# Performance work log

Hardware: AMD Instinct MI355X
Metric: run time of the kernel (lower is better)

## Reference

```python
import jax, jax.numpy as jnp
import numpy as np

N_NODES = 50000
N_EDGES = 800000
HIDDEN = 128
HEADS = 4
LAYERS = 2
NEG_SLOPE = 0.2


def setup_inputs() -> dict:
    key = jax.random.key(0)
    ks = jax.random.split(key, 12)
    s_in = 1.0 / np.sqrt(HIDDEN)
    x = jax.random.normal(ks[0], (N_NODES, HIDDEN), dtype=jnp.float32)
    edge_index = jax.random.randint(ks[1], (2, N_EDGES), 0, N_NODES, dtype=jnp.int64)
    conv_w = jax.random.normal(ks[2], (LAYERS, HIDDEN, HEADS * HIDDEN), dtype=jnp.float32) * s_in
    att_src = jax.random.normal(ks[3], (LAYERS, HEADS, HIDDEN), dtype=jnp.float32) * s_in
    att_dst = jax.random.normal(ks[4], (LAYERS, HEADS, HIDDEN), dtype=jnp.float32) * s_in
    conv_b = jax.random.normal(ks[5], (LAYERS, HIDDEN), dtype=jnp.float32) * 0.01
    proj_w = jax.random.normal(ks[6], (LAYERS, HIDDEN, HIDDEN), dtype=jnp.float32) * s_in
    proj_b = jax.random.normal(ks[7], (LAYERS, HIDDEN), dtype=jnp.float32) * 0.01
    skip_w = jax.random.normal(ks[8], (LAYERS, HIDDEN, HIDDEN), dtype=jnp.float32) * s_in
    skip_b = jax.random.normal(ks[9], (LAYERS, HIDDEN), dtype=jnp.float32) * 0.01
    return {"x": x, "edge_index": edge_index, "conv_w": conv_w, "att_src": att_src,
            "att_dst": att_dst, "conv_b": conv_b, "proj_w": proj_w, "proj_b": proj_b,
            "skip_w": skip_w, "skip_b": skip_b}


def _gat_layer(x, src, dst, W, a_s, a_d, b):
    # x: [N, D]; W: [D, H*C]; a_s, a_d: [H, C]; b: [C]
    N = x.shape[0]
    h = (x @ W).reshape(N, HEADS, HIDDEN)          # [N, H, C]
    alpha_src = jnp.einsum('nhc,hc->nh', h, a_s)   # [N, H]
    alpha_dst = jnp.einsum('nhc,hc->nh', h, a_d)   # [N, H]
    alpha = alpha_src[src] + alpha_dst[dst]        # [E, H]
    alpha = jnp.where(alpha >= 0, alpha, NEG_SLOPE * alpha)  # leaky_relu(0.2)
    amax = jax.ops.segment_max(alpha, dst, num_segments=N)   # [N, H]
    ex = jnp.exp(alpha - amax[dst])                # [E, H]
    denom = jax.ops.segment_sum(ex, dst, num_segments=N)     # [N, H]
    w = ex / (denom[dst] + 1e-16)                  # PyG softmax eps
    msg = h[src] * w[:, :, None]                   # [E, H, C]
    out = jax.ops.segment_sum(msg, dst, num_segments=N)      # [N, H, C]
    return out.mean(axis=1) + b                    # concat=False -> head mean


def reference(x, edge_index, conv_w, att_src, att_dst, conv_b, proj_w, proj_b, skip_w, skip_b):
    src, dst = edge_index[0], edge_index[1]
    out = x
    for l in range(LAYERS):
        conv = _gat_layer(out, src, dst, conv_w[l], att_src[l], att_dst[l], conv_b[l])
        out = jax.nn.relu(conv) @ proj_w[l] + proj_b[l] + (out @ skip_w[l] + skip_b[l])
    return out
```

## Files before the change

kernel.cpp:

```cpp
#include <hip/hip_runtime.h>
#include <hip/hip_bf16.h>
#include <stdint.h>

#define N_NODES 50000
#define N_EDGES 800000
#define HIDDEN  128
#define HEADS   4
#define HD      (HEADS*HIDDEN)
#define CAST_Q  (N_NODES*HIDDEN/4)
#define NTILES  (N_NODES/16)

#define NBUCK   196
#define TILE_H  8192
#define NBLK_H  ((N_EDGES + TILE_H - 1) / TILE_H)
#define NBH     (NBUCK * NBLK_H)
#define SWZ_N   196608
#define HIST_B0 ((CAST_Q + SWZ_N) / 256)

typedef __attribute__((ext_vector_type(8))) short  short8;
typedef __attribute__((ext_vector_type(4))) float  floatx4;
typedef __attribute__((ext_vector_type(2))) float  floatx2;

static __device__ __forceinline__ unsigned short bf16_bits(float f) {
    __hip_bfloat16 h = __float2bfloat16(f);
    union { __hip_bfloat16 b; unsigned short s; } u; u.b = h; return u.s;
}

static __device__ __forceinline__ float lexp(float a) {
    return __expf(fmaxf(a, 0.2f * a));
}


#if __has_builtin(__builtin_amdgcn_cvt_pk_fp8_f32) && __has_builtin(__builtin_amdgcn_cvt_pk_f32_fp8)
#define FP8_HW 1
#else
#define FP8_HW 0
static __device__ __forceinline__ unsigned fp8_enc1(float f) {
    unsigned s = __float_as_uint(f) >> 31;
    float a = fabsf(f);
    if (a < 0.0009765625f) return s << 7;
    if (a > 448.f) a = 448.f;
    unsigned ub = __float_as_uint(a) + 0x00080000u;
    int e = (int)((ub >> 23) & 255) - 120;
    unsigned m = (ub >> 20) & 7;
    if (e <= 0) {
        int mm = (int)(a * 512.f + 0.5f); if (mm > 7) mm = 7;
        return (s << 7) | (unsigned)mm;
    }
    if (e > 15) { e = 15; m = 7; }
    return (s << 7) | ((unsigned)e << 3) | m;
}
static __device__ __forceinline__ floatx2 fp8_dec_pk(unsigned b2) {
    floatx2 r;
    unsigned b = b2 & 255;
    {
        unsigned s = (b >> 7) & 1, e = (b >> 3) & 15, m = b & 7;
        r.x = (e == 0) ? ((s ? -1.f : 1.f) * (float)m * 0.001953125f)
                       : __uint_as_float((s << 31) | ((e + 120) << 23) | (m << 20));
    }
    b = (b2 >> 8) & 255;
    {
        unsigned s = (b >> 7) & 1, e = (b >> 3) & 15, m = b & 7;
        r.y = (e == 0) ? ((s ? -1.f : 1.f) * (float)m * 0.001953125f)
                       : __uint_as_float((s << 31) | ((e + 120) << 23) | (m << 20));
    }
    return r;
}
#endif

static __device__ __forceinline__ unsigned fp8_pack4(float a, float b, float c, float d) {
#if FP8_HW
    int w = __builtin_amdgcn_cvt_pk_fp8_f32(a, b, 0, false);
    w     = __builtin_amdgcn_cvt_pk_fp8_f32(c, d, w, true);
    return (unsigned)w;
#else
    return fp8_enc1(a) | (fp8_enc1(b) << 8) | (fp8_enc1(c) << 16) | (fp8_enc1(d) << 24);
#endif
}

static __device__ __forceinline__ void accf8p(floatx2* acc2, uint2 u, float wt) {
    floatx2 wv = {wt, wt};
#if FP8_HW
    acc2[0] += wv * __builtin_amdgcn_cvt_pk_f32_fp8((int)u.x, false);
    acc2[1] += wv * __builtin_amdgcn_cvt_pk_f32_fp8((int)u.x, true);
    acc2[2] += wv * __builtin_amdgcn_cvt_pk_f32_fp8((int)u.y, false);
    acc2[3] += wv * __builtin_amdgcn_cvt_pk_f32_fp8((int)u.y, true);
#else
    acc2[0] += wv * fp8_dec_pk(u.x);
    acc2[1] += wv * fp8_dec_pk(u.x >> 16);
    acc2[2] += wv * fp8_dec_pk(u.y);
    acc2[3] += wv * fp8_dec_pk(u.y >> 16);
#endif
}


__global__ __launch_bounds__(256) void prep_k(
        const float* __restrict__ x, unsigned short* __restrict__ xb16,
        const float* __restrict__ conv_w, const float* __restrict__ proj_w,
        const float* __restrict__ skip_w,
        unsigned short* __restrict__ cwb, unsigned short* __restrict__ pwb,
        unsigned short* __restrict__ swb,
        const int* __restrict__ dst, int* __restrict__ bh) {
    __shared__ int hh[NBUCK];
    if (blockIdx.x >= HIST_B0) {
        int blk = blockIdx.x - HIST_B0;
        for (int c = threadIdx.x; c < NBUCK; c += 256) hh[c] = 0;
        __syncthreads();
        int e0 = blk * TILE_H;
#pragma unroll
        for (int i = 0; i < TILE_H / 256; ++i) {
            int e = e0 + threadIdx.x + i * 256;
            if (e < N_EDGES) atomicAdd(&hh[dst[e] >> 8], 1);
        }
        __syncthreads();
        for (int c = threadIdx.x; c < NBUCK; c += 256) bh[c * NBLK_H + blk] = hh[c];
        return;
    }
    int i = blockIdx.x * 256 + threadIdx.x;
    if (i < CAST_Q) {
        float4 v = ((const float4*)x)[i];
        uint2 p;
        p.x = (unsigned)bf16_bits(v.x) | ((unsigned)bf16_bits(v.y) << 16);
        p.y = (unsigned)bf16_bits(v.z) | ((unsigned)bf16_bits(v.w) << 16);
        ((uint2*)xb16)[i] = p;
        return;
    }
    int o = i - CAST_Q;
    const float* B; unsigned short* D; int off, N; bool perm = false;
    if (o < 131072)      { B = conv_w + (o >> 16) * 65536; D = cwb + (o >> 16) * 65536; off = o & 65535; N = 512; }
    else if (o < 163840) { int t = o - 131072; B = proj_w + (t >> 14) * 16384; D = pwb + (t >> 14) * 16384; off = t & 16383; N = 128; perm = true; }
    else                 { int t = o - 163840; B = skip_w + (t >> 14) * 16384; D = swb + (t >> 14) * 16384; off = t & 16383; N = 128; }
    int j = off & 7, r = (off >> 3) & 15, q = (off >> 7) & 3;
    int rest = off >> 9, ntn = N >> 4;
    int nt = rest % ntn, kc = rest / ntn;
    int kr = kc * 32 + q * 8 + j;
    int row = perm ? ((kr & 7) * 16 + (kr >> 3)) : kr;
    D[off] = bf16_bits(B[(size_t)row * N + nt * 16 + r]);
}


#define SCAN_PT ((NBH + 1023) / 1024)

__global__ __launch_bounds__(1024) void scanA_k(int* __restrict__ bh) {
    __shared__ int buf[1024];
    int t = threadIdx.x;
    int base = t * SCAN_PT;
    int loc[SCAN_PT];
    int s = 0;
#pragma unroll
    for (int i = 0; i < SCAN_PT; ++i) {
        int idx = base + i;
        int v = (idx < NBH) ? bh[idx] : 0;
        loc[i] = s; s += v;
    }
    buf[t] = s;
    __syncthreads();
    for (int off = 1; off < 1024; off <<= 1) {
        int xv = (t >= off) ? buf[t - off] : 0;
        __syncthreads();
        buf[t] += xv;
        __syncthreads();
    }
    int excl = buf[t] - s;
#pragma unroll
    for (int i = 0; i < SCAN_PT; ++i) {
        int idx = base + i;
        if (idx < NBH) bh[idx] = excl + loc[i];
    }
}


__global__ __launch_bounds__(256) void scatterA_k(const int* __restrict__ src,
                                                  const int* __restrict__ dst,
                                                  const int* __restrict__ bh,
                                                  unsigned* __restrict__ tmp) {
    __shared__ int cnt[NBUCK];
    int t = threadIdx.x, blk = blockIdx.x;
    for (int c = t; c < NBUCK; c += 256) cnt[c] = bh[c * NBLK_H + blk];
    __syncthreads();
    int e0 = blk * TILE_H;
#pragma unroll
    for (int i = 0; i < TILE_H / 256; ++i) {
        int e = e0 + t + i * 256;
        if (e < N_EDGES) {
            int d = dst[e];
            int pos = atomicAdd(&cnt[d >> 8], 1);
            tmp[pos] = ((unsigned)(d & 255) << 16) | (unsigned)src[e];
        }
    }
}


__global__ __launch_bounds__(256) void sortB_k(const unsigned* __restrict__ tmp,
                                               const int* __restrict__ bh,
                                               int* __restrict__ src_sorted,
                                               int* __restrict__ row_ptr) {
    __shared__ int cnt[256], buf[256], pos[256];
    int t = threadIdx.x, b = blockIdx.x;
    int beg = bh[b * NBLK_H];
    int end = (b == NBUCK - 1) ? N_EDGES : bh[(b + 1) * NBLK_H];
    cnt[t] = 0;
    __syncthreads();
    for (int i = beg + t; i < end; i += 256) atomicAdd(&cnt[(tmp[i] >> 16) & 255], 1);
    __syncthreads();
    int v = cnt[t];
    buf[t] = v;
    __syncthreads();
    for (int off = 1; off < 256; off <<= 1) {
        int xv = (t >= off) ? buf[t - off] : 0;
        __syncthreads();
        buf[t] += xv;
        __syncthreads();
    }
    int excl = buf[t] - v;
    int d = b * 256 + t;
    if (d <= N_NODES) row_ptr[d] = beg + excl;
    pos[t] = excl;
    __syncthreads();
    for (int i = beg + t; i < end; i += 256) {
        unsigned w = tmp[i];
        int c = (w >> 16) & 255;
        int p = beg + atomicAdd(&pos[c], 1);
        src_sorted[p] = (int)(w & 0xFFFFu);
    }
}


__global__ __launch_bounds__(256, 2) void gemmc_k(
        const __hip_bfloat16* __restrict__ A,
        const unsigned short* __restrict__ Bs,
        const float* __restrict__ att_s, const float* __restrict__ att_d,
        unsigned char* __restrict__ h8,
        float* __restrict__ a_src, float* __restrict__ a_dst, int mtiles) {
    int head = threadIdx.x >> 6;
    int lane = threadIdx.x & 63;
    int r = lane & 15, q = lane >> 4;

    short8 Bf[4][8];
#pragma unroll
    for (int kc = 0; kc < 4; ++kc)
#pragma unroll
        for (int ntl = 0; ntl < 8; ++ntl)
            Bf[kc][ntl] = *(const short8*)((const short*)Bs +
                (((size_t)(kc * 32 + head * 8 + ntl) * 4 + q) * 128 + r * 8));

    float as_r[8], ad_r[8];
#pragma unroll
    for (int ntl = 0; ntl < 8; ++ntl) {
        as_r[ntl] = att_s[head * HIDDEN + ntl * 16 + r];
        ad_r[ntl] = att_d[head * HIDDEN + ntl * 16 + r];
    }

    const int stride = gridDim.x;
    int mt = blockIdx.x;
    short8 av[4];
    if (mt < mtiles) {
        const short* Ab = (const short*)A + (size_t)(mt * 16 + r) * HIDDEN + q * 8;
#pragma unroll
        for (int kc = 0; kc < 4; ++kc) av[kc] = *(const short8*)(Ab + kc * 32);
    }
    while (mt < mtiles) {
        int nmt = mt + stride;
        short8 avn[4];
        if (nmt < mtiles) {
            const short* Ab = (const short*)A + (size_t)(nmt * 16 + r) * HIDDEN + q * 8;
#pragma unroll
            for (int kc = 0; kc < 4; ++kc) avn[kc] = *(const short8*)(Ab + kc * 32);
        }
        int m0 = mt * 16;
        floatx4 acc[8];
#pragma unroll
        for (int i = 0; i < 8; ++i) acc[i] = (floatx4){0.f, 0.f, 0.f, 0.f};
#pragma unroll
        for (int kc = 0; kc < 4; ++kc)
#pragma unroll
            for (int ntl = 0; ntl < 8; ++ntl)
                acc[ntl] = __builtin_amdgcn_mfma_f32_16x16x32_bf16(av[kc], Bf[kc][ntl], acc[ntl], 0, 0, 0);

#pragma unroll
        for (int i = 0; i < 4; ++i) {
            uint2 o;
            o.x = fp8_pack4(acc[0][i], acc[1][i], acc[2][i], acc[3][i]);
            o.y = fp8_pack4(acc[4][i], acc[5][i], acc[6][i], acc[7][i]);
            *(uint2*)(h8 + (size_t)(m0 + q * 4 + i) * HD + head * HIDDEN + r * 8) = o;
        }
        float sA[4] = {0, 0, 0, 0}, sD[4] = {0, 0, 0, 0};
#pragma unroll
        for (int ntl = 0; ntl < 8; ++ntl)
#pragma unroll
            for (int i = 0; i < 4; ++i) {
                sA[i] += acc[ntl][i] * as_r[ntl];
                sD[i] += acc[ntl][i] * ad_r[ntl];
            }
#pragma unroll
        for (int d = 1; d < 16; d <<= 1)
#pragma unroll
            for (int i = 0; i < 4; ++i) {
                sA[i] += __shfl_xor(sA[i], d);
                sD[i] += __shfl_xor(sD[i], d);
            }
        if (r == 0)
#pragma unroll
            for (int i = 0; i < 4; ++i) {
                int row = m0 + q * 4 + i;
                a_src[row * HEADS + head] = sA[i];
                a_dst[row * HEADS + head] = sD[i];
            }
        mt = nmt;
#pragma unroll
        for (int kc = 0; kc < 4; ++kc) av[kc] = avn[kc];
    }
}


template <typename OutT>
__global__ __launch_bounds__(256, 2) void gemmp_k(
        const __hip_bfloat16* __restrict__ A,  const unsigned short* __restrict__ Bs,
        const __hip_bfloat16* __restrict__ A2, const unsigned short* __restrict__ Bs2,
        const float* __restrict__ b1, const float* __restrict__ b2,
        OutT* __restrict__ D, int mtiles) {
    int wave = threadIdx.x >> 6;
    int lane = threadIdx.x & 63;
    int r = lane & 15, q = lane >> 4;
    int nh = wave & 1;

    short8 Bf[4][4], Bf2[4][4];
#pragma unroll
    for (int kc = 0; kc < 4; ++kc)
#pragma unroll
        for (int ntl = 0; ntl < 4; ++ntl) {
            size_t off = (((size_t)(kc * 8 + nh * 4 + ntl) * 4 + q) * 128 + r * 8);
            Bf[kc][ntl]  = *(const short8*)((const short*)Bs  + off);
            Bf2[kc][ntl] = *(const short8*)((const short*)Bs2 + off);
        }
    float bias[4];
#pragma unroll
    for (int ntl = 0; ntl < 4; ++ntl) {
        int col = nh * 64 + ntl * 16 + r;
        bias[ntl] = b1[col] + b2[col];
    }

    const int stride = gridDim.x * 2;
    int mt = blockIdx.x * 2 + (wave >> 1);
    short8 av[4], av2[4];
    if (mt < mtiles) {
        const short* Ab  = (const short*)A  + (size_t)(mt * 16 + r) * HIDDEN + q * 8;
        const short* Ab2 = (const short*)A2 + (size_t)(mt * 16 + r) * HIDDEN + q * 8;
#pragma unroll
        for (int kc = 0; kc < 4; ++kc) {
            av[kc]  = *(const short8*)(Ab  + kc * 32);
            av2[kc] = *(const short8*)(Ab2 + kc * 32);
        }
    }
    while (mt < mtiles) {
        int nmt = mt + stride;
        short8 avn[4], avn2[4];
        if (nmt < mtiles) {
            const short* Ab  = (const short*)A  + (size_t)(nmt * 16 + r) * HIDDEN + q * 8;
            const short* Ab2 = (const short*)A2 + (size_t)(nmt * 16 + r) * HIDDEN + q * 8;
#pragma unroll
            for (int kc = 0; kc < 4; ++kc) {
                avn[kc]  = *(const short8*)(Ab  + kc * 32);
                avn2[kc] = *(const short8*)(Ab2 + kc * 32);
            }
        }
        int m0 = mt * 16;
        floatx4 acc[4];
#pragma unroll
        for (int i = 0; i < 4; ++i) acc[i] = (floatx4){0.f, 0.f, 0.f, 0.f};
#pragma unroll
        for (int kc = 0; kc < 4; ++kc)
#pragma unroll
            for (int ntl = 0; ntl < 4; ++ntl) {
                acc[ntl] = __builtin_amdgcn_mfma_f32_16x16x32_bf16(av[kc],  Bf[kc][ntl],  acc[ntl], 0, 0, 0);
                acc[ntl] = __builtin_amdgcn_mfma_f32_16x16x32_bf16(av2[kc], Bf2[kc][ntl], acc[ntl], 0, 0, 0);
            }
#pragma unroll
        for (int ntl = 0; ntl < 4; ++ntl) {
            int col = nh * 64 + ntl * 16 + r;
#pragma unroll
            for (int i = 0; i < 4; ++i) {
                int row = m0 + q * 4 + i;
                float v = acc[ntl][i] + bias[ntl];
                if constexpr (sizeof(OutT) == 4)
                    ((float*)D)[(size_t)row * HIDDEN + col] = v;
                else
                    ((__hip_bfloat16*)D)[(size_t)row * HIDDEN + col] = __float2bfloat16(v);
            }
        }
        mt = nmt;
#pragma unroll
        for (int kc = 0; kc < 4; ++kc) { av[kc] = avn[kc]; av2[kc] = avn2[kc]; }
    }
}


__global__ __launch_bounds__(256) void msg_k(const int* __restrict__ row_ptr,
                                             const int* __restrict__ src_sorted,
                                             const float* __restrict__ a_src,
                                             const float* __restrict__ a_dst,
                                             const unsigned char* __restrict__ h8,
                                             const float* __restrict__ conv_b,
                                             __hip_bfloat16* __restrict__ rc) {
    int wave = threadIdx.x >> 6;
    int lane = threadIdx.x & 63;
    int n = blockIdx.x * 4 + wave;
    if (n >= N_NODES) return;
    int head = lane >> 4;
    float adn = a_dst[n * HEADS + head];
    int beg = row_ptr[n], end = row_ptr[n + 1];
    const uint2* hq = (const uint2*)h8;

    floatx2 acc2[4];
#pragma unroll
    for (int k = 0; k < 4; ++k) acc2[k] = (floatx2){0.f, 0.f};
    float esum = 0.f;
    for (int base = beg; base < end; base += 32) {
        int m = min(32, end - base);
        int sv = (lane < m) ? src_sorted[base + lane] : 0;
        int j = 0;
        for (; j + 4 <= m; j += 4) {
            int s0 = __shfl(sv, j),     s1 = __shfl(sv, j + 1);
            int s2 = __shfl(sv, j + 2), s3 = __shfl(sv, j + 3);
            uint2 u0 = hq[(size_t)s0 * 64 + lane];
            uint2 u1 = hq[(size_t)s1 * 64 + lane];
            uint2 u2 = hq[(size_t)s2 * 64 + lane];
            uint2 u3 = hq[(size_t)s3 * 64 + lane];
            float e0 = lexp(a_src[s0 * 4 + head] + adn);
            float e1 = lexp(a_src[s1 * 4 + head] + adn);
            float e2 = lexp(a_src[s2 * 4 + head] + adn);
            float e3 = lexp(a_src[s3 * 4 + head] + adn);
            accf8p(acc2, u0, e0);
            accf8p(acc2, u1, e1);
            accf8p(acc2, u2, e2);
            accf8p(acc2, u3, e3);
            esum += (e0 + e1) + (e2 + e3);
        }
        for (; j < m; ++j) {
            int s0 = __shfl(sv, j);
            uint2 u0 = hq[(size_t)s0 * 64 + lane];
            float e0 = lexp(a_src[s0 * 4 + head] + adn);
            accf8p(acc2, u0, e0);
            esum += e0;
        }
    }
    float rinv = 1.f / (esum + 1e-16f);
    float acc[8];
#pragma unroll
    for (int k = 0; k < 4; ++k) { acc[2 * k] = acc2[k].x * rinv; acc[2 * k + 1] = acc2[k].y * rinv; }
#pragma unroll
    for (int k = 0; k < 8; ++k) {
        acc[k] += __shfl_xor(acc[k], 16);
        acc[k] += __shfl_xor(acc[k], 32);
    }
    if (lane < 16) {
        union { uint4 v; unsigned short us[8]; } o;
#pragma unroll
        for (int k = 0; k < 8; ++k) {
            float mres = 0.25f * acc[k] + conv_b[k * 16 + lane];
            o.us[k] = bf16_bits(mres > 0.f ? mres : 0.f);
        }
        ((uint4*)rc)[(size_t)n * 16 + lane] = o.v;
    }
}


extern "C" void kernel_launch(void* const* d_in, const int* in_sizes, int n_in,
                              void* d_out, int out_size, void* d_ws, size_t ws_size,
                              hipStream_t stream) {
    const float* x      = (const float*)d_in[0];
    const int*   ei     = (const int*)d_in[1];
    const float* conv_w = (const float*)d_in[2];
    const float* att_s  = (const float*)d_in[3];
    const float* att_d  = (const float*)d_in[4];
    const float* conv_b = (const float*)d_in[5];
    const float* proj_w = (const float*)d_in[6];
    const float* proj_b = (const float*)d_in[7];
    const float* skip_w = (const float*)d_in[8];
    const float* skip_b = (const float*)d_in[9];
    float* out = (float*)d_out;

    char* ws = (char*)d_ws;
    size_t o = 0;
    auto alloc = [&](size_t b) { size_t c = o; o += (b + 255) & ~(size_t)255; return c; };
    __hip_bfloat16* xb16 = (__hip_bfloat16*)(ws + alloc((size_t)N_NODES * HIDDEN * 2));
    unsigned short* cwb  = (unsigned short*)(ws + alloc((size_t)2 * HIDDEN * HD * 2));
    unsigned short* pwb  = (unsigned short*)(ws + alloc((size_t)2 * HIDDEN * HIDDEN * 2));
    unsigned short* swb  = (unsigned short*)(ws + alloc((size_t)2 * HIDDEN * HIDDEN * 2));
    unsigned char* h8    = (unsigned char*)(ws + alloc((size_t)N_NODES * HD));
    float* a_src         = (float*)(ws + alloc((size_t)N_NODES * HEADS * 4));
    float* a_dst         = (float*)(ws + alloc((size_t)N_NODES * HEADS * 4));
    int* row_ptr         = (int*)(ws + alloc((size_t)(N_NODES + 1) * 4));
    int* src_s           = (int*)(ws + alloc((size_t)N_EDGES * 4));
    __hip_bfloat16* rc   = (__hip_bfloat16*)(ws + alloc((size_t)N_NODES * HIDDEN * 2));
    __hip_bfloat16* xb   = (__hip_bfloat16*)(ws + alloc((size_t)N_NODES * HIDDEN * 2));
    int* bh              = (int*)(ws + alloc((size_t)NBH * 4));

    unsigned* tmp = (unsigned*)rc;

    const int* srcp = ei;
    const int* dstp = ei + N_EDGES;

    prep_k<<<HIST_B0 + NBLK_H, 256, 0, stream>>>(
        x, (unsigned short*)xb16, conv_w, proj_w, skip_w, cwb, pwb, swb, dstp, bh);
    scanA_k<<<1, 1024, 0, stream>>>(bh);
    scatterA_k<<<NBLK_H, 256, 0, stream>>>(srcp, dstp, bh, tmp);
    sortB_k<<<NBUCK, 256, 0, stream>>>(tmp, bh, src_s, row_ptr);

    const __hip_bfloat16* xc = xb16;
    for (int l = 0; l < 2; ++l) {
        gemmc_k<<<512, 256, 0, stream>>>(
            xc, cwb + (size_t)l * HIDDEN * HD,
            att_s + l * HD, att_d + l * HD, h8, a_src, a_dst, NTILES);
        msg_k<<<(N_NODES + 3) / 4, 256, 0, stream>>>(
            row_ptr, src_s, a_src, a_dst, h8, conv_b + l * HIDDEN, rc);
        if (l == 0)
            gemmp_k<__hip_bfloat16><<<512, 256, 0, stream>>>(
                rc, pwb + (size_t)l * HIDDEN * HIDDEN,
                xc, swb + (size_t)l * HIDDEN * HIDDEN,
                proj_b + l * HIDDEN, skip_b + l * HIDDEN, xb, NTILES);
        else
            gemmp_k<float><<<512, 256, 0, stream>>>(
                rc, pwb + (size_t)l * HIDDEN * HIDDEN,
                xc, swb + (size_t)l * HIDDEN * HIDDEN,
                proj_b + l * HIDDEN, skip_b + l * HIDDEN, out, NTILES);
        xc = xb;
    }
}
```

Before: 331.2 us.

## Fuse bucket scan and scatter into layer-0 GEMM launch, use readlane in msg

Removes the single-block scan kernel. Each scatter block now computes its own bucket offsets by summing histogram rows, and sortB recomputes bucket bounds the same way. These scatter blocks run as extra blocks in the same launch as the layer-0 conv GEMM, so edge sorting overlaps with the GEMM and launches drop. msg_k uses readlane instead of shfl to broadcast source indices. The cost is redundant histogram re-reading in every scatter and sort block.

```diff
diff --git a/kernel.cpp b/kernel.cpp
--- a/kernel.cpp
+++ b/kernel.cpp
@@ -16,6 +16,7 @@
 #define NBH     (NBUCK * NBLK_H)
 #define SWZ_N   196608
 #define HIST_B0 ((CAST_Q + SWZ_N) / 256)
+#define GEMM_BLKS 512
 
 typedef __attribute__((ext_vector_type(8))) short  short8;
 typedef __attribute__((ext_vector_type(4))) float  floatx4;
@@ -139,44 +140,133 @@
 }
 
 
-#define SCAN_PT ((NBH + 1023) / 1024)
-
-__global__ __launch_bounds__(1024) void scanA_k(int* __restrict__ bh) {
-    __shared__ int buf[1024];
+static __device__ __forceinline__ void gemmc_body(
+        const __hip_bfloat16* __restrict__ A, const unsigned short* __restrict__ Bs,
+        const float* __restrict__ att_s, const float* __restrict__ att_d,
+        unsigned char* __restrict__ h8,
+        float* __restrict__ a_src, float* __restrict__ a_dst,
+        int mtiles, int bid, int stride) {
+    int head = threadIdx.x >> 6;
+    int lane = threadIdx.x & 63;
+    int r = lane & 15, q = lane >> 4;
+
+    short8 Bf[4][8];
+#pragma unroll
+    for (int kc = 0; kc < 4; ++kc)
+#pragma unroll
+        for (int ntl = 0; ntl < 8; ++ntl)
+            Bf[kc][ntl] = *(const short8*)((const short*)Bs +
+                (((size_t)(kc * 32 + head * 8 + ntl) * 4 + q) * 128 + r * 8));
+
+    float as_r[8], ad_r[8];
+#pragma unroll
+    for (int ntl = 0; ntl < 8; ++ntl) {
+        as_r[ntl] = att_s[head * HIDDEN + ntl * 16 + r];
+        ad_r[ntl] = att_d[head * HIDDEN + ntl * 16 + r];
+    }
+
+    int mt = bid;
+    short8 av[4];
+    if (mt < mtiles) {
+        const short* Ab = (const short*)A + (size_t)(mt * 16 + r) * HIDDEN + q * 8;
+#pragma unroll
+        for (int kc = 0; kc < 4; ++kc) av[kc] = *(const short8*)(Ab + kc * 32);
+    }
+    while (mt < mtiles) {
+        int nmt = mt + stride;
+        short8 avn[4];
+        if (nmt < mtiles) {
+            const short* Ab = (const short*)A + (size_t)(nmt * 16 + r) * HIDDEN + q * 8;
+#pragma unroll
+            for (int kc = 0; kc < 4; ++kc) avn[kc] = *(const short8*)(Ab + kc * 32);
+        }
+        int m0 = mt * 16;
+        floatx4 acc[8];
+#pragma unroll
+        for (int i = 0; i < 8; ++i) acc[i] = (floatx4){0.f, 0.f, 0.f, 0.f};
+#pragma unroll
+        for (int kc = 0; kc < 4; ++kc)
+#pragma unroll
+            for (int ntl = 0; ntl < 8; ++ntl)
+                acc[ntl] = __builtin_amdgcn_mfma_f32_16x16x32_bf16(av[kc], Bf[kc][ntl], acc[ntl], 0, 0, 0);
+
+#pragma unroll
+        for (int i = 0; i < 4; ++i) {
+            uint2 o;
+            o.x = fp8_pack4(acc[0][i], acc[1][i], acc[2][i], acc[3][i]);
+            o.y = fp8_pack4(acc[4][i], acc[5][i], acc[6][i], acc[7][i]);
+            *(uint2*)(h8 + (size_t)(m0 + q * 4 + i) * HD + head * HIDDEN + r * 8) = o;
+        }
+        float sA[4] = {0, 0, 0, 0}, sD[4] = {0, 0, 0, 0};
+#pragma unroll
+        for (int ntl = 0; ntl < 8; ++ntl)
+#pragma unroll
+            for (int i = 0; i < 4; ++i) {
+                sA[i] += acc[ntl][i] * as_r[ntl];
+                sD[i] += acc[ntl][i] * ad_r[ntl];
+            }
+#pragma unroll
+        for (int d = 1; d < 16; d <<= 1)
+#pragma unroll
+            for (int i = 0; i < 4; ++i) {
+                sA[i] += __shfl_xor(sA[i], d);
+                sD[i] += __shfl_xor(sD[i], d);
+            }
+        if (r == 0)
+#pragma unroll
+            for (int i = 0; i < 4; ++i) {
+                int row = m0 + q * 4 + i;
+                a_src[row * HEADS + head] = sA[i];
+                a_dst[row * HEADS + head] = sD[i];
+            }
+        mt = nmt;
+#pragma unroll
+        for (int kc = 0; kc < 4; ++kc) av[kc] = avn[kc];
+    }
+}
+
+__global__ __launch_bounds__(256, 2) void gemmc_k(
+        const __hip_bfloat16* __restrict__ A, const unsigned short* __restrict__ Bs,
+        const float* __restrict__ att_s, const float* __restrict__ att_d,
+        unsigned char* __restrict__ h8,
+        float* __restrict__ a_src, float* __restrict__ a_dst, int mtiles) {
+    gemmc_body(A, Bs, att_s, att_d, h8, a_src, a_dst, mtiles, blockIdx.x, gridDim.x);
+}
+
+
+__global__ __launch_bounds__(256, 2) void gemmcsc_k(
+        const __hip_bfloat16* __restrict__ A, const unsigned short* __restrict__ Bs,
+        const float* __restrict__ att_s, const float* __restrict__ att_d,
+        unsigned char* __restrict__ h8,
+        float* __restrict__ a_src, float* __restrict__ a_dst, int mtiles,
+        const int* __restrict__ src, const int* __restrict__ dst,
+        const int* __restrict__ bh, unsigned* __restrict__ tmp) {
+    __shared__ int cnt[256], scanbuf[256];
+    if (blockIdx.x < GEMM_BLKS) {
+        gemmc_body(A, Bs, att_s, att_d, h8, a_src, a_dst, mtiles, blockIdx.x, GEMM_BLKS);
+        return;
+    }
+    int blk = blockIdx.x - GEMM_BLKS;
     int t = threadIdx.x;
-    int base = t * SCAN_PT;
-    int loc[SCAN_PT];
-    int s = 0;
-#pragma unroll
-    for (int i = 0; i < SCAN_PT; ++i) {
-        int idx = base + i;
-        int v = (idx < NBH) ? bh[idx] : 0;
-        loc[i] = s; s += v;
-    }
-    buf[t] = s;
-    __syncthreads();
-    for (int off = 1; off < 1024; off <<= 1) {
-        int xv = (t >= off) ? buf[t - off] : 0;
-        __syncthreads();
-        buf[t] += xv;
-        __syncthreads();
-    }
-    int excl = buf[t] - s;
-#pragma unroll
-    for (int i = 0; i < SCAN_PT; ++i) {
-        int idx = base + i;
-        if (idx < NBH) bh[idx] = excl + loc[i];
-    }
-}
-
-
-__global__ __launch_bounds__(256) void scatterA_k(const int* __restrict__ src,
-                                                  const int* __restrict__ dst,
-                                                  const int* __restrict__ bh,
-                                                  unsigned* __restrict__ tmp) {
-    __shared__ int cnt[NBUCK];
-    int t = threadIdx.x, blk = blockIdx.x;
-    for (int c = t; c < NBUCK; c += 256) cnt[c] = bh[c * NBLK_H + blk];
+    int Tt = 0, Pt = 0;
+    if (t < NBUCK) {
+        const int* row = bh + (size_t)t * NBLK_H;
+        for (int i = 0; i < NBLK_H; ++i) {
+            int v = row[i];
+            Tt += v;
+            Pt += (i < blk) ? v : 0;
+        }
+    }
+    scanbuf[t] = Tt;
+    __syncthreads();
+    for (int off = 1; off < 256; off <<= 1) {
+        int xv = (t >= off) ? scanbuf[t - off] : 0;
+        __syncthreads();
+        scanbuf[t] += xv;
+        __syncthreads();
+    }
+    int excl = scanbuf[t] - Tt;
+    if (t < NBUCK) cnt[t] = excl + Pt;
     __syncthreads();
     int e0 = blk * TILE_H;
 #pragma unroll
@@ -195,10 +285,26 @@
                                                const int* __restrict__ bh,
                                                int* __restrict__ src_sorted,
                                                int* __restrict__ row_ptr) {
-    __shared__ int cnt[256], buf[256], pos[256];
+    __shared__ int cnt[256], buf[256], pos[256], bbase[256], btot[256];
     int t = threadIdx.x, b = blockIdx.x;
-    int beg = bh[b * NBLK_H];
-    int end = (b == NBUCK - 1) ? N_EDGES : bh[(b + 1) * NBLK_H];
+    int Tt = 0;
+    if (t < NBUCK) {
+        const int* row = bh + (size_t)t * NBLK_H;
+        for (int i = 0; i < NBLK_H; ++i) Tt += row[i];
+    }
+    buf[t] = Tt;
+    __syncthreads();
+    for (int off = 1; off < 256; off <<= 1) {
+        int xv = (t >= off) ? buf[t - off] : 0;
+        __syncthreads();
+        buf[t] += xv;
+        __syncthreads();
+    }
+    bbase[t] = buf[t] - Tt;
+    btot[t]  = Tt;
+    __syncthreads();
+    int beg = bbase[b];
+    int end = beg + btot[b];
     cnt[t] = 0;
     __syncthreads();
     for (int i = beg + t; i < end; i += 256) atomicAdd(&cnt[(tmp[i] >> 16) & 255], 1);
@@ -222,93 +328,6 @@
         int c = (w >> 16) & 255;
         int p = beg + atomicAdd(&pos[c], 1);
         src_sorted[p] = (int)(w & 0xFFFFu);
-    }
-}
-
-
-__global__ __launch_bounds__(256, 2) void gemmc_k(
-        const __hip_bfloat16* __restrict__ A,
-        const unsigned short* __restrict__ Bs,
-        const float* __restrict__ att_s, const float* __restrict__ att_d,
-        unsigned char* __restrict__ h8,
-        float* __restrict__ a_src, float* __restrict__ a_dst, int mtiles) {
-    int head = threadIdx.x >> 6;
-    int lane = threadIdx.x & 63;
-    int r = lane & 15, q = lane >> 4;
-
-    short8 Bf[4][8];
-#pragma unroll
-    for (int kc = 0; kc < 4; ++kc)
-#pragma unroll
-        for (int ntl = 0; ntl < 8; ++ntl)
-            Bf[kc][ntl] = *(const short8*)((const short*)Bs +
-                (((size_t)(kc * 32 + head * 8 + ntl) * 4 + q) * 128 + r * 8));
-
-    float as_r[8], ad_r[8];
-#pragma unroll
-    for (int ntl = 0; ntl < 8; ++ntl) {
-        as_r[ntl] = att_s[head * HIDDEN + ntl * 16 + r];
-        ad_r[ntl] = att_d[head * HIDDEN + ntl * 16 + r];
-    }
-
-    const int stride = gridDim.x;
-    int mt = blockIdx.x;
-    short8 av[4];
-    if (mt < mtiles) {
-        const short* Ab = (const short*)A + (size_t)(mt * 16 + r) * HIDDEN + q * 8;
-#pragma unroll
-        for (int kc = 0; kc < 4; ++kc) av[kc] = *(const short8*)(Ab + kc * 32);
-    }
-    while (mt < mtiles) {
-        int nmt = mt + stride;
-        short8 avn[4];
-        if (nmt < mtiles) {
-            const short* Ab = (const short*)A + (size_t)(nmt * 16 + r) * HIDDEN + q * 8;
-#pragma unroll
-            for (int kc = 0; kc < 4; ++kc) avn[kc] = *(const short8*)(Ab + kc * 32);
-        }
-        int m0 = mt * 16;
-        floatx4 acc[8];
-#pragma unroll
-        for (int i = 0; i < 8; ++i) acc[i] = (floatx4){0.f, 0.f, 0.f, 0.f};
-#pragma unroll
-        for (int kc = 0; kc < 4; ++kc)
-#pragma unroll
-            for (int ntl = 0; ntl < 8; ++ntl)
-                acc[ntl] = __builtin_amdgcn_mfma_f32_16x16x32_bf16(av[kc], Bf[kc][ntl], acc[ntl], 0, 0, 0);
-
-#pragma unroll
-        for (int i = 0; i < 4; ++i) {
-            uint2 o;
-            o.x = fp8_pack4(acc[0][i], acc[1][i], acc[2][i], acc[3][i]);
-            o.y = fp8_pack4(acc[4][i], acc[5][i], acc[6][i], acc[7][i]);
-            *(uint2*)(h8 + (size_t)(m0 + q * 4 + i) * HD + head * HIDDEN + r * 8) = o;
-        }
-        float sA[4] = {0, 0, 0, 0}, sD[4] = {0, 0, 0, 0};
-#pragma unroll
-        for (int ntl = 0; ntl < 8; ++ntl)
-#pragma unroll
-            for (int i = 0; i < 4; ++i) {
-                sA[i] += acc[ntl][i] * as_r[ntl];
-                sD[i] += acc[ntl][i] * ad_r[ntl];
-            }
-#pragma unroll
-        for (int d = 1; d < 16; d <<= 1)
-#pragma unroll
-            for (int i = 0; i < 4; ++i) {
-                sA[i] += __shfl_xor(sA[i], d);
-                sD[i] += __shfl_xor(sD[i], d);
-            }
-        if (r == 0)
-#pragma unroll
-            for (int i = 0; i < 4; ++i) {
-                int row = m0 + q * 4 + i;
-                a_src[row * HEADS + head] = sA[i];
-                a_dst[row * HEADS + head] = sD[i];
-            }
-        mt = nmt;
-#pragma unroll
-        for (int kc = 0; kc < 4; ++kc) av[kc] = avn[kc];
     }
 }
 
@@ -420,8 +439,10 @@
         int sv = (lane < m) ? src_sorted[base + lane] : 0;
         int j = 0;
         for (; j + 4 <= m; j += 4) {
-            int s0 = __shfl(sv, j),     s1 = __shfl(sv, j + 1);
-            int s2 = __shfl(sv, j + 2), s3 = __shfl(sv, j + 3);
+            int s0 = __builtin_amdgcn_readlane(sv, j);
+            int s1 = __builtin_amdgcn_readlane(sv, j + 1);
+            int s2 = __builtin_amdgcn_readlane(sv, j + 2);
+            int s3 = __builtin_amdgcn_readlane(sv, j + 3);
             uint2 u0 = hq[(size_t)s0 * 64 + lane];
             uint2 u1 = hq[(size_t)s1 * 64 + lane];
             uint2 u2 = hq[(size_t)s2 * 64 + lane];
@@ -437,7 +458,7 @@
             esum += (e0 + e1) + (e2 + e3);
         }
         for (; j < m; ++j) {
-            int s0 = __shfl(sv, j);
+            int s0 = __builtin_amdgcn_readlane(sv, j);
             uint2 u0 = hq[(size_t)s0 * 64 + lane];
             float e0 = lexp(a_src[s0 * 4 + head] + adn);
             accf8p(acc2, u0, e0);
@@ -503,27 +524,24 @@
 
     prep_k<<<HIST_B0 + NBLK_H, 256, 0, stream>>>(
         x, (unsigned short*)xb16, conv_w, proj_w, skip_w, cwb, pwb, swb, dstp, bh);
-    scanA_k<<<1, 1024, 0, stream>>>(bh);
-    scatterA_k<<<NBLK_H, 256, 0, stream>>>(srcp, dstp, bh, tmp);
+
+    gemmcsc_k<<<GEMM_BLKS + NBLK_H, 256, 0, stream>>>(
+        xb16, cwb, att_s, att_d, h8, a_src, a_dst, NTILES,
+        srcp, dstp, bh, tmp);
     sortB_k<<<NBUCK, 256, 0, stream>>>(tmp, bh, src_s, row_ptr);
 
-    const __hip_bfloat16* xc = xb16;
-    for (int l = 0; l < 2; ++l) {
-        gemmc_k<<<512, 256, 0, stream>>>(
-            xc, cwb + (size_t)l * HIDDEN * HD,
-            att_s + l * HD, att_d + l * HD, h8, a_src, a_dst, NTILES);
-        msg_k<<<(N_NODES + 3) / 4, 256, 0, stream>>>(
-            row_ptr, src_s, a_src, a_dst, h8, conv_b + l * HIDDEN, rc);
-        if (l == 0)
-            gemmp_k<__hip_bfloat16><<<512, 256, 0, stream>>>(
-                rc, pwb + (size_t)l * HIDDEN * HIDDEN,
-                xc, swb + (size_t)l * HIDDEN * HIDDEN,
-                proj_b + l * HIDDEN, skip_b + l * HIDDEN, xb, NTILES);
-        else
-            gemmp_k<float><<<512, 256, 0, stream>>>(
-                rc, pwb + (size_t)l * HIDDEN * HIDDEN,
-                xc, swb + (size_t)l * HIDDEN * HIDDEN,
-                proj_b + l * HIDDEN, skip_b + l * HIDDEN, out, NTILES);
-        xc = xb;
-    }
-}
+    msg_k<<<(N_NODES + 3) / 4, 256, 0, stream>>>(
+        row_ptr, src_s, a_src, a_dst, h8, conv_b, rc);
+    gemmp_k<__hip_bfloat16><<<512, 256, 0, stream>>>(
+        rc, pwb, xb16, swb, proj_b, skip_b, xb, NTILES);
+
+    gemmc_k<<<512, 256, 0, stream>>>(
+        xb, cwb + (size_t)HIDDEN * HD,
+        att_s + HD, att_d + HD, h8, a_src, a_dst, NTILES);
+    msg_k<<<(N_NODES + 3) / 4, 256, 0, stream>>>(
+        row_ptr, src_s, a_src, a_dst, h8, conv_b + HIDDEN, rc);
+    gemmp_k<float><<<512, 256, 0, stream>>>(
+        rc, pwb + (size_t)HIDDEN * HIDDEN,
+        xb, swb + (size_t)HIDDEN * HIDDEN,
+        proj_b + HIDDEN, skip_b + HIDDEN, out, NTILES);
+}
```

After: 313.0 us. 5.5% less time.
